# Kernel optimization log

Measured on AMD Instinct MI355X. Metric: run time of the kernel, lower is better.

The kernel has to match this reference:

```python
import jax, jax.numpy as jnp
import numpy as np

IN_DIM = 1024
OUT_DIM = 1024
NHEAD = 16
K = 9  # template(1032) - dim(1024) + 1


def _slinear(vec, template, conv_w, conv_b, lin_b):
    # Conv2d over template produces the [out_dim, in_dim] weight matrix.
    w = jax.lax.conv_general_dilated(
        template, conv_w, window_strides=(1, 1), padding='VALID',
        dimension_numbers=('NCHW', 'OIHW', 'NCHW'))  # [1,1,out_dim,in_dim]
    w = w[0, 0] + conv_b  # broadcast conv bias (scalar per out-channel)
    return vec @ w.T + lin_b  # F.linear(vec, w) + bias


def setup_inputs() -> dict:
    key = jax.random.key(0)
    ks = jax.random.split(key, 13)
    S, B = 2048, 2
    d = {
        'query': jax.random.normal(ks[0], (S, B, IN_DIM), jnp.float32),
        'key': jax.random.normal(ks[1], (S, B, IN_DIM), jnp.float32),
        'value': jax.random.normal(ks[2], (S, B, IN_DIM), jnp.float32),
        'template': jax.random.normal(ks[3], (1, 1, 1032, 1032), jnp.float32),
    }
    for i, name in enumerate(['wq', 'wk', 'wv']):
        d[name + '_cw'] = jax.random.normal(ks[4 + 3 * i], (1, 1, K, K), jnp.float32) * 0.05
        d[name + '_cb'] = jax.random.normal(ks[5 + 3 * i], (1,), jnp.float32) * 0.05
        d[name + '_b'] = jax.random.normal(ks[6 + 3 * i], (OUT_DIM,), jnp.float32) * 0.05
    return d


def reference(query, key, value, template,
              wq_cw, wq_cb, wq_b, wk_cw, wk_cb, wk_b, wv_cw, wv_cb, wv_b):
    q = _slinear(query, template, wq_cw, wq_cb, wq_b)
    k = _slinear(key, template, wk_cw, wk_cb, wk_b)
    v = _slinear(value, template, wv_cw, wv_cb, wv_b)
    S, B = q.shape[0], q.shape[1]
    h_dim = OUT_DIM // NHEAD
    scale = h_dim ** 0.5
    qh = q.reshape(S, B, NHEAD, h_dim)
    kh = k.reshape(S, B, NHEAD, h_dim)
    vh = v.reshape(S, B, NHEAD, h_dim)
    # batch_first=False path: scores then softmax over last dim
    scores = jnp.einsum('ibhd,jbhd->bhij', qh, kh) / scale  # [B,H,S,S]
    attn = jax.nn.softmax(scores, axis=-1)
    out = jnp.einsum('bhij,jbhd->ibhd', attn, vh).reshape(S, B, OUT_DIM)
    return out
```

## Files before the change

### kernel.cpp

```cpp
#include <hip/hip_runtime.h>
#include <math.h>

#define TDIM   1032
#define DIM    1024
#define SLEN   2048
#define BATCH  2
#define NROWS  (SLEN*BATCH)
#define NHEAD  16
#define HD     64

typedef unsigned short u16;
typedef short short8 __attribute__((ext_vector_type(8)));
typedef short bf16x4 __attribute__((ext_vector_type(4)));
typedef float f32x4  __attribute__((ext_vector_type(4)));

#define CSCALE 0.18033688011112042f

__device__ inline unsigned fbits(float x) {
    union { float f; unsigned u; } v; v.f = x; return v.u;
}
__device__ inline float asfloat(unsigned u) {
    union { unsigned u; float f; } v; v.u = u; return v.f;
}
__device__ inline u16 f2bf_rne(float x) {
    unsigned u = fbits(x);
    unsigned r = u + 0x7fffu + ((u >> 16) & 1u);
    return (u16)(r >> 16);
}
__device__ inline float bf2f(u16 b) { return asfloat(((unsigned)b) << 16); }
__device__ inline void dma16(const u16* g, u16* l) {
    __builtin_amdgcn_global_load_lds(
        (const __attribute__((address_space(1))) void*)g,
        (__attribute__((address_space(3))) void*)l, 16, 0, 0);
}

__global__ __launch_bounds__(256) void conv_weight_kernel(
    const float* __restrict__ tmpl,
    const float* __restrict__ cw0, const float* __restrict__ cb0,
    const float* __restrict__ cw1, const float* __restrict__ cb1,
    const float* __restrict__ cw2, const float* __restrict__ cb2,
    u16* __restrict__ Wh, u16* __restrict__ Wl)
{
    int t = blockIdx.z;
    const float* cw = (t == 0) ? cw0 : ((t == 1) ? cw1 : cw2);
    const float* cb = (t == 0) ? cb0 : ((t == 1) ? cb1 : cb2);
    __shared__ float scw[81];
    if (threadIdx.x < 81) scw[threadIdx.x] = cw[threadIdx.x];
    __syncthreads();
    int i = blockIdx.x * 256 + threadIdx.x;
    int o4 = blockIdx.y * 4;
    float cbv = cb[0];
    float acc[4] = {cbv, cbv, cbv, cbv};
    #pragma unroll
    for (int ry = 0; ry < 12; ++ry) {
        const float* trow = tmpl + (size_t)(o4 + ry) * TDIM + i;
        float tv[9];
        #pragma unroll
        for (int dx = 0; dx < 9; ++dx) tv[dx] = trow[dx];
        #pragma unroll
        for (int oo = 0; oo < 4; ++oo) {
            int dy = ry - oo;
            if (dy >= 0 && dy <= 8) {
                #pragma unroll
                for (int dx = 0; dx < 9; ++dx)
                    acc[oo] = fmaf(scw[dy * 9 + dx], tv[dx], acc[oo]);
            }
        }
    }
    #pragma unroll
    for (int oo = 0; oo < 4; ++oo) {
        size_t idx = (size_t)t * DIM * DIM + (size_t)(o4 + oo) * DIM + i;
        u16 h = f2bf_rne(acc[oo]);
        Wh[idx] = h;
        Wl[idx] = f2bf_rne(acc[oo] - bf2f(h));
    }
}

__global__ __launch_bounds__(256) void xsplit_kernel(
    const float* __restrict__ x0, const float* __restrict__ x1,
    const float* __restrict__ x2,
    u16* __restrict__ Xh, u16* __restrict__ Xl)
{
    int t = blockIdx.y;
    const float* X = (t == 0) ? x0 : ((t == 1) ? x1 : x2);
    u16* oh = Xh + (size_t)t * NROWS * DIM;
    u16* ol = Xl + (size_t)t * NROWS * DIM;
    size_t base = ((size_t)blockIdx.x * 256 + threadIdx.x) * 8;
    float4 a = *(const float4*)(X + base);
    float4 b = *(const float4*)(X + base + 4);
    float v[8] = {a.x, a.y, a.z, a.w, b.x, b.y, b.z, b.w};
    short8 hv, lv;
    #pragma unroll
    for (int e = 0; e < 8; ++e) {
        unsigned u = fbits(v[e]);
        hv[e] = (short)(u >> 16);
        float l = v[e] - asfloat(u & 0xffff0000u);
        lv[e] = (short)(fbits(l) >> 16);
    }
    *(short8*)(oh + base) = hv;
    *(short8*)(ol + base) = lv;
}

__global__ __launch_bounds__(256, 3) void qkv_mfma_gemm_ps(
    const u16* __restrict__ Xhg, const u16* __restrict__ Xlg,
    const u16* __restrict__ Whg, const u16* __restrict__ Wlg,
    const float* __restrict__ b0, const float* __restrict__ b1,
    const float* __restrict__ b2,
    u16* __restrict__ Qh, u16* __restrict__ Ql,
    u16* __restrict__ Kh, u16* __restrict__ Kl,
    u16* __restrict__ Vb)
{
    unsigned flat = blockIdx.x + 8u * blockIdx.y + 256u * blockIdx.z;
    unsigned swz = (flat & 7u) * 96u + (flat >> 3);
    int t = swz >> 8;
    int n0 = (swz & 7u) * 128;
    int m0 = ((swz >> 3) & 31u) * 128;

    const u16* Ah_g = Xhg + (size_t)t * NROWS * DIM;
    const u16* Al_g = Xlg + (size_t)t * NROWS * DIM;
    const u16* Bh_g = Whg + (size_t)t * DIM * DIM;
    const u16* Bl_g = Wlg + (size_t)t * DIM * DIM;
    const float* bias = (t == 0) ? b0 : ((t == 1) ? b1 : b2);

    __shared__ __align__(16) u16 lds[16384];
    u16* sAh = lds;
    u16* sAl = lds + 4096;
    u16* sBh = lds + 8192;
    u16* sBl = lds + 12288;

    int tid = threadIdx.x;
    int w = tid >> 6, lane = tid & 63;
    int c = lane & 15, quad = lane >> 4;
    int mh = (w >> 1) * 64, nh = (w & 1) * 64;

    int srow = lane >> 2, sgr = lane & 3;
    int ssw = sgr ^ ((srow >> 1) & 3);

    f32x4 acc[4][4];
    #pragma unroll
    for (int i = 0; i < 4; ++i)
        #pragma unroll
        for (int j = 0; j < 4; ++j)
            #pragma unroll
            for (int r = 0; r < 4; ++r) acc[i][j][r] = 0.0f;

    float bias_v[4];
    #pragma unroll
    for (int tn = 0; tn < 4; ++tn) bias_v[tn] = bias[n0 + nh + tn * 16 + c];

    #define STAGE(kg) do {                                                     \
        _Pragma("unroll")                                                      \
        for (int i_ = 0; i_ < 2; ++i_) {                                       \
            int rb = w * 32 + i_ * 16;                                         \
            size_t ro = (size_t)(n0 + rb + srow) * DIM + ((kg) + ssw) * 8;     \
            dma16(Bh_g + ro, sBh + rb * 32);                                   \
            dma16(Bl_g + ro, sBl + rb * 32);                                   \
            size_t ao = (size_t)(m0 + rb + srow) * DIM + ((kg) + ssw) * 8;     \
            dma16(Ah_g + ao, sAh + rb * 32);                                   \
            dma16(Al_g + ao, sAl + rb * 32);                                   \
        }                                                                      \
    } while (0)

    STAGE(0);

    for (int it = 0; it < 32; ++it) {
        __syncthreads();

        short8 ah[4], al[4], bh[4], bl[4];
        int rsw = (quad ^ ((c >> 1) & 3)) * 8;
        #pragma unroll
        for (int tt = 0; tt < 4; ++tt) {
            int mi = (mh + tt * 16 + c) * 32 + rsw;
            ah[tt] = *(short8*)(sAh + mi);
            al[tt] = *(short8*)(sAl + mi);
            int ni = (nh + tt * 16 + c) * 32 + rsw;
            bh[tt] = *(short8*)(sBh + ni);
            bl[tt] = *(short8*)(sBl + ni);
        }
        __syncthreads();

        if (it < 31) STAGE((it + 1) * 4);

        #pragma unroll
        for (int tm = 0; tm < 4; ++tm)
            #pragma unroll
            for (int tn = 0; tn < 4; ++tn) {
                acc[tm][tn] = __builtin_amdgcn_mfma_f32_16x16x32_bf16(
                    ah[tm], bh[tn], acc[tm][tn], 0, 0, 0);
                acc[tm][tn] = __builtin_amdgcn_mfma_f32_16x16x32_bf16(
                    ah[tm], bl[tn], acc[tm][tn], 0, 0, 0);
                acc[tm][tn] = __builtin_amdgcn_mfma_f32_16x16x32_bf16(
                    al[tm], bh[tn], acc[tm][tn], 0, 0, 0);
            }
    }
    #undef STAGE

    if (t < 2) {
        u16* Yh = (t == 0) ? Qh : Kh;
        u16* Yl = (t == 0) ? Ql : Kl;
        float qs = (t == 0) ? CSCALE : 1.0f;
        #pragma unroll
        for (int tm = 0; tm < 4; ++tm)
            #pragma unroll
            for (int r = 0; r < 4; ++r) {
                int m = m0 + mh + tm * 16 + quad * 4 + r;
                #pragma unroll
                for (int tn = 0; tn < 4; ++tn) {
                    int n = n0 + nh + tn * 16 + c;
                    float o = (acc[tm][tn][r] + bias_v[tn]) * qs;
                    unsigned bo = fbits(o);
                    Yh[(size_t)m * DIM + n] = (u16)(bo >> 16);
                    float l = o - asfloat(bo & 0xffff0000u);
                    Yl[(size_t)m * DIM + n] = (u16)(fbits(l) >> 16);
                }
            }
    } else {
        #pragma unroll
        for (int tm = 0; tm < 4; ++tm)
            #pragma unroll
            for (int r = 0; r < 4; ++r) {
                int m = m0 + mh + tm * 16 + quad * 4 + r;
                #pragma unroll
                for (int tn = 0; tn < 4; ++tn) {
                    int n = n0 + nh + tn * 16 + c;
                    Vb[(size_t)m * DIM + n] =
                        (u16)(fbits(acc[tm][tn][r] + bias_v[tn]) >> 16);
                }
            }
    }
}

__global__ __launch_bounds__(256, 3) void qkv_mfma_gemm_fb(
    const float* __restrict__ x0, const float* __restrict__ x1,
    const float* __restrict__ x2,
    const u16* __restrict__ Whg, const u16* __restrict__ Wlg,
    const float* __restrict__ b0, const float* __restrict__ b1,
    const float* __restrict__ b2,
    u16* __restrict__ Qh, u16* __restrict__ Ql,
    u16* __restrict__ Kh, u16* __restrict__ Kl,
    u16* __restrict__ Vb)
{
    unsigned flat = blockIdx.x + 8u * blockIdx.y + 256u * blockIdx.z;
    unsigned swz = (flat & 7u) * 96u + (flat >> 3);
    int t = swz >> 8;
    int n0 = (swz & 7u) * 128;
    int m0 = ((swz >> 3) & 31u) * 128;

    const float* X    = (t == 0) ? x0 : ((t == 1) ? x1 : x2);
    const u16* Bh_g   = Whg + (size_t)t * DIM * DIM;
    const u16* Bl_g   = Wlg + (size_t)t * DIM * DIM;
    const float* bias = (t == 0) ? b0 : ((t == 1) ? b1 : b2);

    __shared__ __align__(16) u16 lds[16384];
    u16* sAh = lds;
    u16* sAl = lds + 4096;
    u16* sBh = lds + 8192;
    u16* sBl = lds + 12288;

    int tid = threadIdx.x;
    int w = tid >> 6, lane = tid & 63;
    int c = lane & 15, quad = lane >> 4;
    int mh = (w >> 1) * 64, nh = (w & 1) * 64;

    int arow = w * 32 + (lane & 31);
    int acol = (lane >> 5) * 16;
    const float* aptr = X + (size_t)(m0 + arow) * DIM + acol;
    int awz = (arow >> 1) & 3;

    int srow = lane >> 2, sgr = lane & 3;
    int bsw = sgr ^ ((srow >> 1) & 3);

    f32x4 acc[4][4];
    #pragma unroll
    for (int i = 0; i < 4; ++i)
        #pragma unroll
        for (int j = 0; j < 4; ++j)
            #pragma unroll
            for (int r = 0; r < 4; ++r) acc[i][j][r] = 0.0f;

    float bias_v[4];
    #pragma unroll
    for (int tn = 0; tn < 4; ++tn) bias_v[tn] = bias[n0 + nh + tn * 16 + c];

    float4 xa[4];
    #pragma unroll
    for (int i = 0; i < 2; ++i) {
        int rb = w * 32 + i * 16;
        const u16* gh = Bh_g + (size_t)(n0 + rb + srow) * DIM + bsw * 8;
        const u16* gl = Bl_g + (size_t)(n0 + rb + srow) * DIM + bsw * 8;
        dma16(gh, sBh + rb * 32);
        dma16(gl, sBl + rb * 32);
    }
    #pragma unroll
    for (int j = 0; j < 4; ++j) xa[j] = *(const float4*)(aptr + j * 4);

    for (int it = 0; it < 32; ++it) {
        #pragma unroll
        for (int g = 0; g < 2; ++g) {
            float v[8] = { xa[2*g].x, xa[2*g].y, xa[2*g].z, xa[2*g].w,
                           xa[2*g+1].x, xa[2*g+1].y, xa[2*g+1].z, xa[2*g+1].w };
            short8 hv, lv;
            #pragma unroll
            for (int e = 0; e < 8; ++e) {
                unsigned u = fbits(v[e]);
                hv[e] = (short)(u >> 16);
                float l = v[e] - asfloat(u & 0xffff0000u);
                lv[e] = (short)(fbits(l) >> 16);
            }
            int chunk = (((lane >> 5) * 2 + g) ^ awz) * 8;
            *(short8*)(sAh + arow * 32 + chunk) = hv;
            *(short8*)(sAl + arow * 32 + chunk) = lv;
        }
        __syncthreads();

        short8 ah[4], al[4], bh[4], bl[4];
        int rsw = (quad ^ ((c >> 1) & 3)) * 8;
        #pragma unroll
        for (int tt = 0; tt < 4; ++tt) {
            int mi = (mh + tt * 16 + c) * 32 + rsw;
            ah[tt] = *(short8*)(sAh + mi);
            al[tt] = *(short8*)(sAl + mi);
            int ni = (nh + tt * 16 + c) * 32 + rsw;
            bh[tt] = *(short8*)(sBh + ni);
            bl[tt] = *(short8*)(sBl + ni);
        }
        __syncthreads();

        if (it < 31) {
            int kg = (it + 1) * 4;
            #pragma unroll
            for (int i = 0; i < 2; ++i) {
                int rb = w * 32 + i * 16;
                const u16* gh = Bh_g + (size_t)(n0 + rb + srow) * DIM + (kg + bsw) * 8;
                const u16* gl = Bl_g + (size_t)(n0 + rb + srow) * DIM + (kg + bsw) * 8;
                dma16(gh, sBh + rb * 32);
                dma16(gl, sBl + rb * 32);
            }
            #pragma unroll
            for (int j = 0; j < 4; ++j)
                xa[j] = *(const float4*)(aptr + (it + 1) * 32 + j * 4);
        }

        #pragma unroll
        for (int tm = 0; tm < 4; ++tm)
            #pragma unroll
            for (int tn = 0; tn < 4; ++tn) {
                acc[tm][tn] = __builtin_amdgcn_mfma_f32_16x16x32_bf16(
                    ah[tm], bh[tn], acc[tm][tn], 0, 0, 0);
                acc[tm][tn] = __builtin_amdgcn_mfma_f32_16x16x32_bf16(
                    ah[tm], bl[tn], acc[tm][tn], 0, 0, 0);
                acc[tm][tn] = __builtin_amdgcn_mfma_f32_16x16x32_bf16(
                    al[tm], bh[tn], acc[tm][tn], 0, 0, 0);
            }
    }

    if (t < 2) {
        u16* Yh = (t == 0) ? Qh : Kh;
        u16* Yl = (t == 0) ? Ql : Kl;
        float qs = (t == 0) ? CSCALE : 1.0f;
        #pragma unroll
        for (int tm = 0; tm < 4; ++tm)
            #pragma unroll
            for (int r = 0; r < 4; ++r) {
                int m = m0 + mh + tm * 16 + quad * 4 + r;
                #pragma unroll
                for (int tn = 0; tn < 4; ++tn) {
                    int n = n0 + nh + tn * 16 + c;
                    float o = (acc[tm][tn][r] + bias_v[tn]) * qs;
                    unsigned bo = fbits(o);
                    Yh[(size_t)m * DIM + n] = (u16)(bo >> 16);
                    float l = o - asfloat(bo & 0xffff0000u);
                    Yl[(size_t)m * DIM + n] = (u16)(fbits(l) >> 16);
                }
            }
    } else {
        #pragma unroll
        for (int tm = 0; tm < 4; ++tm)
            #pragma unroll
            for (int r = 0; r < 4; ++r) {
                int m = m0 + mh + tm * 16 + quad * 4 + r;
                #pragma unroll
                for (int tn = 0; tn < 4; ++tn) {
                    int n = n0 + nh + tn * 16 + c;
                    Vb[(size_t)m * DIM + n] =
                        (u16)(fbits(acc[tm][tn][r] + bias_v[tn]) >> 16);
                }
            }
    }
}

__global__ __launch_bounds__(256) void vt_kernel(
    const u16* __restrict__ Vb, u16* __restrict__ Vt)
{
    int b = blockIdx.z, h = blockIdx.y, s0 = blockIdx.x * 64;
    __shared__ __align__(16) u16 tile[64][80];
    int tid = threadIdx.x;
    int sl = tid >> 2, d0 = (tid & 3) * 16;
    const u16* src = Vb + (size_t)((s0 + sl) * BATCH + b) * DIM + h * HD + d0;
    short8 v0 = *(const short8*)src;
    short8 v1 = *(const short8*)(src + 8);
    #pragma unroll
    for (int j = 0; j < 8; ++j) {
        tile[d0 + j][sl] = (u16)v0[j];
        tile[d0 + 8 + j][sl] = (u16)v1[j];
    }
    __syncthreads();
    int d = tid >> 2, sc0 = (tid & 3) * 16;
    u16* dst = Vt + (size_t)((b * NHEAD + h) * HD + d) * SLEN + s0 + sc0;
    *(short8*)dst = *(const short8*)&tile[d][sc0];
    *(short8*)(dst + 8) = *(const short8*)&tile[d][sc0 + 8];
}

__global__ __launch_bounds__(512, 4) void attn_mfma_kernel(
    const u16* __restrict__ Qh, const u16* __restrict__ Ql,
    const u16* __restrict__ Kh, const u16* __restrict__ Kl,
    const u16* __restrict__ Vt, float* __restrict__ out)
{
    unsigned flat = blockIdx.x + 16u * blockIdx.y + 256u * blockIdx.z;
    unsigned swz = (flat & 7u) * 64u + (flat >> 3);
    int q0 = (swz & 15u) * 128;
    int h = (swz >> 4) & 15u;
    int b = swz >> 8;

    int tid = threadIdx.x;
    int w = tid >> 6, lane = tid & 63;
    int c = lane & 15, quad = lane >> 4;

    __shared__ __align__(16) u16 sbuf[2][3][4096];
    __shared__ __align__(16) u16 sP[8][1024];

    short8 qhf[2], qlf[2];
    {
        int s = q0 + w * 16 + c;
        size_t base = (size_t)(s * BATCH + b) * DIM + h * HD + quad * 8;
        qhf[0] = *(const short8*)(Qh + base);
        qhf[1] = *(const short8*)(Qh + base + 32);
        qlf[0] = *(const short8*)(Ql + base);
        qlf[1] = *(const short8*)(Ql + base + 32);
    }

    f32x4 acc[4];
    #pragma unroll
    for (int i = 0; i < 4; ++i)
        #pragma unroll
        for (int r = 0; r < 4; ++r) acc[i][r] = 0.0f;
    float m_run = -1e38f, l_run = 0.0f;

    int r3 = lane >> 3, c3 = lane & 7;
    int sw = c3 ^ r3;
    const size_t bhofs = (size_t)(b * NHEAD + h) * HD;

    #define ISSUE_DMA(n0v, bufv) do {                                          \
        int row_ = w * 8 + r3;                                                 \
        size_t gk = (size_t)(((n0v) + row_) * BATCH + b) * DIM + h * HD + sw * 8; \
        dma16(Kh + gk, &sbuf[bufv][0][w * 512]);                               \
        dma16(Kl + gk, &sbuf[bufv][1][w * 512]);                               \
        size_t gv = (bhofs + row_) * SLEN + (n0v) + sw * 8;                    \
        dma16(Vt + gv, &sbuf[bufv][2][w * 512]);                               \
    } while (0)

    ISSUE_DMA(0, 0);

    for (int it = 0; it < 32; ++it) {
        int cur = it & 1;
        __syncthreads();
        if (it < 31) ISSUE_DMA((it + 1) * 64, cur ^ 1);

        const u16* bKh = sbuf[cur][0];
        const u16* bKl = sbuf[cur][1];
        const u16* bVt = sbuf[cur][2];

        f32x4 sc[4];
        #pragma unroll
        for (int ct = 0; ct < 4; ++ct) {
            int row = ct * 16 + c, rw = row & 7;
            int kb = row * 64;
            short8 kh0 = *(const short8*)(bKh + kb + ((quad ^ rw) * 8));
            short8 kh1 = *(const short8*)(bKh + kb + (((4 + quad) ^ rw) * 8));
            short8 kl0 = *(const short8*)(bKl + kb + ((quad ^ rw) * 8));
            short8 kl1 = *(const short8*)(bKl + kb + (((4 + quad) ^ rw) * 8));
            __builtin_amdgcn_s_setprio(1);
            f32x4 s = {0.0f, 0.0f, 0.0f, 0.0f};
            s = __builtin_amdgcn_mfma_f32_16x16x32_bf16(kh0, qhf[0], s, 0, 0, 0);
            s = __builtin_amdgcn_mfma_f32_16x16x32_bf16(kh1, qhf[1], s, 0, 0, 0);
            s = __builtin_amdgcn_mfma_f32_16x16x32_bf16(kh0, qlf[0], s, 0, 0, 0);
            s = __builtin_amdgcn_mfma_f32_16x16x32_bf16(kh1, qlf[1], s, 0, 0, 0);
            s = __builtin_amdgcn_mfma_f32_16x16x32_bf16(kl0, qhf[0], s, 0, 0, 0);
            s = __builtin_amdgcn_mfma_f32_16x16x32_bf16(kl1, qhf[1], s, 0, 0, 0);
            __builtin_amdgcn_s_setprio(0);
            sc[ct] = s;
        }

        short8 vv[4][2];
        #pragma unroll
        for (int ctd = 0; ctd < 4; ++ctd) {
            int vrow = ctd * 16 + c, vrw = vrow & 7;
            int vb = vrow * 64;
            vv[ctd][0] = *(const short8*)(bVt + vb + ((quad ^ vrw) * 8));
            vv[ctd][1] = *(const short8*)(bVt + vb + (((4 + quad) ^ vrw) * 8));
        }

        u16* wp = sP[w];
        short8 pf0, pf1;
        {
            float m00 = fmaxf(fmaxf(sc[0][0], sc[0][1]), fmaxf(sc[0][2], sc[0][3]));
            float m01 = fmaxf(fmaxf(sc[1][0], sc[1][1]), fmaxf(sc[1][2], sc[1][3]));
            float m10 = fmaxf(fmaxf(sc[2][0], sc[2][1]), fmaxf(sc[2][2], sc[2][3]));
            float m11 = fmaxf(fmaxf(sc[3][0], sc[3][1]), fmaxf(sc[3][2], sc[3][3]));
            float pm = fmaxf(fmaxf(m00, m01), fmaxf(m10, m11));
            pm = fmaxf(pm, __shfl_xor(pm, 16));
            pm = fmaxf(pm, __shfl_xor(pm, 32));
            float mnew = fmaxf(m_run, pm);
            bool noresc = __all(pm <= m_run);
            if (!noresc) {
                float al = exp2f(m_run - mnew);
                float alr[4];
                #pragma unroll
                for (int r = 0; r < 4; ++r)
                    alr[r] = __shfl(al, (lane & 48) | (quad * 4 + r));
                #pragma unroll
                for (int ctd = 0; ctd < 4; ++ctd)
                    #pragma unroll
                    for (int r = 0; r < 4; ++r) acc[ctd][r] *= alr[r];
                l_run *= al;
            }
            m_run = mnew;

            float psp[4];
            int prow = c * 64;
            #pragma unroll
            for (int ct = 0; ct < 4; ++ct) {
                float p0 = exp2f(sc[ct][0] - mnew);
                float p1 = exp2f(sc[ct][1] - mnew);
                float p2 = exp2f(sc[ct][2] - mnew);
                float p3 = exp2f(sc[ct][3] - mnew);
                psp[ct] = (p0 + p1) + (p2 + p3);
                bf16x4 pk;
                pk[0] = (short)(fbits(p0) >> 16);
                pk[1] = (short)(fbits(p1) >> 16);
                pk[2] = (short)(fbits(p2) >> 16);
                pk[3] = (short)(fbits(p3) >> 16);
                int phys = (ct * 2 + (quad >> 1)) ^ (c & 7);
                *(bf16x4*)(wp + prow + phys * 8 + (quad & 1) * 4) = pk;
            }
            float ps = (psp[0] + psp[1]) + (psp[2] + psp[3]);
            ps += __shfl_xor(ps, 16);
            ps += __shfl_xor(ps, 32);
            l_run += ps;

            int rw = c & 7;
            pf0 = *(const short8*)(wp + prow + ((quad ^ rw) * 8));
            pf1 = *(const short8*)(wp + prow + (((4 + quad) ^ rw) * 8));
        }

        __builtin_amdgcn_s_setprio(1);
        #pragma unroll
        for (int ctd = 0; ctd < 4; ++ctd) {
            acc[ctd] = __builtin_amdgcn_mfma_f32_16x16x32_bf16(
                pf0, vv[ctd][0], acc[ctd], 0, 0, 0);
            acc[ctd] = __builtin_amdgcn_mfma_f32_16x16x32_bf16(
                pf1, vv[ctd][1], acc[ctd], 0, 0, 0);
        }
        __builtin_amdgcn_s_setprio(0);
    }
    #undef ISSUE_DMA

    {
        float rl[4];
        #pragma unroll
        for (int r = 0; r < 4; ++r)
            rl[r] = 1.0f / __shfl(l_run, (lane & 48) | (quad * 4 + r));
        #pragma unroll
        for (int ctd = 0; ctd < 4; ++ctd)
            #pragma unroll
            for (int r = 0; r < 4; ++r) {
                int s = q0 + w * 16 + quad * 4 + r;
                out[(size_t)(s * BATCH + b) * DIM + h * HD + ctd * 16 + c] =
                    acc[ctd][r] * rl[r];
            }
    }
}

extern "C" void kernel_launch(void* const* d_in, const int* in_sizes, int n_in,
                              void* d_out, int out_size, void* d_ws, size_t ws_size,
                              hipStream_t stream)
{
    const float* query = (const float*)d_in[0];
    const float* key_  = (const float*)d_in[1];
    const float* value = (const float*)d_in[2];
    const float* tmpl  = (const float*)d_in[3];
    const float* wq_cw = (const float*)d_in[4];
    const float* wq_cb = (const float*)d_in[5];
    const float* wq_b  = (const float*)d_in[6];
    const float* wk_cw = (const float*)d_in[7];
    const float* wk_cb = (const float*)d_in[8];
    const float* wk_b  = (const float*)d_in[9];
    const float* wv_cw = (const float*)d_in[10];
    const float* wv_cb = (const float*)d_in[11];
    const float* wv_b  = (const float*)d_in[12];

    char* ws = (char*)d_ws;
    u16* Wh = (u16*)(ws);
    u16* Wl = (u16*)(ws + 6291456);
    u16* Qh = (u16*)(ws + 12582912);
    u16* Ql = (u16*)(ws + 20971520);
    u16* Kh = (u16*)(ws + 29360128);
    u16* Kl = (u16*)(ws + 37748736);
    u16* Vb = (u16*)(ws + 46137344);
    u16* Vt = (u16*)(ws + 54525952);
    u16* Xh = (u16*)(ws + 62914560);
    u16* Xl = (u16*)(ws + 88080384);
    float* out = (float*)d_out;

    bool presplit = ws_size >= 113246208ull;

    conv_weight_kernel<<<dim3(DIM / 256, DIM / 4, 3), 256, 0, stream>>>(
        tmpl, wq_cw, wq_cb, wk_cw, wk_cb, wv_cw, wv_cb, Wh, Wl);

    if (presplit) {
        xsplit_kernel<<<dim3(NROWS * DIM / (256 * 8), 3), 256, 0, stream>>>(
            query, key_, value, Xh, Xl);
        qkv_mfma_gemm_ps<<<dim3(DIM / 128, NROWS / 128, 3), 256, 0, stream>>>(
            Xh, Xl, Wh, Wl, wq_b, wk_b, wv_b, Qh, Ql, Kh, Kl, Vb);
    } else {
        qkv_mfma_gemm_fb<<<dim3(DIM / 128, NROWS / 128, 3), 256, 0, stream>>>(
            query, key_, value, Wh, Wl, wq_b, wk_b, wv_b, Qh, Ql, Kh, Kl, Vb);
    }

    vt_kernel<<<dim3(SLEN / 64, NHEAD, BATCH), 256, 0, stream>>>(Vb, Vt);

    attn_mfma_kernel<<<dim3(SLEN / 128, NHEAD, BATCH), 512, 0, stream>>>(
        Qh, Ql, Kh, Kl, Vt, out);
}
```

Baseline: 300.3 us.

## Process two query sub-tiles per warp in attention to reuse K/V fragments

Each warp now handles 32 query rows (two 16-row sub-tiles) instead of 16, so the attention block covers 256 queries and the grid halves. Every K and V fragment loaded from shared memory, and every K/V DMA tile, now feeds twice as many MFMAs. This cuts K/V traffic per query and doubles per-warp instruction-level parallelism. In exchange, register use roughly doubles for accumulators, scores and Q fragments, launch bounds drop to 2 blocks per CU, and there are only 256 blocks for the GPU's CUs.

Result: slower. 314.9 us (+4.9%).

```diff
diff --git a/kernel.cpp b/kernel.cpp
--- a/kernel.cpp
+++ b/kernel.cpp
@@ -411,40 +411,43 @@
     *(short8*)(dst + 8) = *(const short8*)&tile[d][sc0 + 8];
 }
 
-__global__ __launch_bounds__(512, 4) void attn_mfma_kernel(
+__global__ __launch_bounds__(512, 2) void attn_mfma_kernel(
     const u16* __restrict__ Qh, const u16* __restrict__ Ql,
     const u16* __restrict__ Kh, const u16* __restrict__ Kl,
     const u16* __restrict__ Vt, float* __restrict__ out)
 {
-    unsigned flat = blockIdx.x + 16u * blockIdx.y + 256u * blockIdx.z;
-    unsigned swz = (flat & 7u) * 64u + (flat >> 3);
-    int q0 = (swz & 15u) * 128;
-    int h = (swz >> 4) & 15u;
-    int b = swz >> 8;
+    unsigned flat = blockIdx.x + 8u * blockIdx.y + 128u * blockIdx.z;
+    unsigned swz = (flat & 7u) * 32u + (flat >> 3);
+    int q0 = (swz & 7u) * 256;
+    int h = (swz >> 3) & 15u;
+    int b = swz >> 7;
 
     int tid = threadIdx.x;
     int w = tid >> 6, lane = tid & 63;
     int c = lane & 15, quad = lane >> 4;
 
     __shared__ __align__(16) u16 sbuf[2][3][4096];
-    __shared__ __align__(16) u16 sP[8][1024];
-
-    short8 qhf[2], qlf[2];
-    {
-        int s = q0 + w * 16 + c;
+    __shared__ __align__(16) u16 sP[8][2048];
+
+    short8 qhf[2][2], qlf[2][2];
+    #pragma unroll
+    for (int u = 0; u < 2; ++u) {
+        int s = q0 + w * 32 + u * 16 + c;
         size_t base = (size_t)(s * BATCH + b) * DIM + h * HD + quad * 8;
-        qhf[0] = *(const short8*)(Qh + base);
-        qhf[1] = *(const short8*)(Qh + base + 32);
-        qlf[0] = *(const short8*)(Ql + base);
-        qlf[1] = *(const short8*)(Ql + base + 32);
-    }
-
-    f32x4 acc[4];
-    #pragma unroll
-    for (int i = 0; i < 4; ++i)
-        #pragma unroll
-        for (int r = 0; r < 4; ++r) acc[i][r] = 0.0f;
-    float m_run = -1e38f, l_run = 0.0f;
+        qhf[u][0] = *(const short8*)(Qh + base);
+        qhf[u][1] = *(const short8*)(Qh + base + 32);
+        qlf[u][0] = *(const short8*)(Ql + base);
+        qlf[u][1] = *(const short8*)(Ql + base + 32);
+    }
+
+    f32x4 acc[2][4];
+    #pragma unroll
+    for (int u = 0; u < 2; ++u)
+        #pragma unroll
+        for (int i = 0; i < 4; ++i)
+            #pragma unroll
+            for (int r = 0; r < 4; ++r) acc[u][i][r] = 0.0f;
+    float m_run[2] = {-1e38f, -1e38f}, l_run[2] = {0.0f, 0.0f};
 
     int r3 = lane >> 3, c3 = lane & 7;
     int sw = c3 ^ r3;
@@ -470,7 +473,7 @@
         const u16* bKl = sbuf[cur][1];
         const u16* bVt = sbuf[cur][2];
 
-        f32x4 sc[4];
+        f32x4 sc[2][4];
         #pragma unroll
         for (int ct = 0; ct < 4; ++ct) {
             int row = ct * 16 + c, rw = row & 7;
@@ -480,15 +483,18 @@
             short8 kl0 = *(const short8*)(bKl + kb + ((quad ^ rw) * 8));
             short8 kl1 = *(const short8*)(bKl + kb + (((4 + quad) ^ rw) * 8));
             __builtin_amdgcn_s_setprio(1);
-            f32x4 s = {0.0f, 0.0f, 0.0f, 0.0f};
-            s = __builtin_amdgcn_mfma_f32_16x16x32_bf16(kh0, qhf[0], s, 0, 0, 0);
-            s = __builtin_amdgcn_mfma_f32_16x16x32_bf16(kh1, qhf[1], s, 0, 0, 0);
-            s = __builtin_amdgcn_mfma_f32_16x16x32_bf16(kh0, qlf[0], s, 0, 0, 0);
-            s = __builtin_amdgcn_mfma_f32_16x16x32_bf16(kh1, qlf[1], s, 0, 0, 0);
-            s = __builtin_amdgcn_mfma_f32_16x16x32_bf16(kl0, qhf[0], s, 0, 0, 0);
-            s = __builtin_amdgcn_mfma_f32_16x16x32_bf16(kl1, qhf[1], s, 0, 0, 0);
+            #pragma unroll
+            for (int u = 0; u < 2; ++u) {
+                f32x4 s = {0.0f, 0.0f, 0.0f, 0.0f};
+                s = __builtin_amdgcn_mfma_f32_16x16x32_bf16(kh0, qhf[u][0], s, 0, 0, 0);
+                s = __builtin_amdgcn_mfma_f32_16x16x32_bf16(kh1, qhf[u][1], s, 0, 0, 0);
+                s = __builtin_amdgcn_mfma_f32_16x16x32_bf16(kh0, qlf[u][0], s, 0, 0, 0);
+                s = __builtin_amdgcn_mfma_f32_16x16x32_bf16(kh1, qlf[u][1], s, 0, 0, 0);
+                s = __builtin_amdgcn_mfma_f32_16x16x32_bf16(kl0, qhf[u][0], s, 0, 0, 0);
+                s = __builtin_amdgcn_mfma_f32_16x16x32_bf16(kl1, qhf[u][1], s, 0, 0, 0);
+                sc[u][ct] = s;
+            }
             __builtin_amdgcn_s_setprio(0);
-            sc[ct] = s;
         }
 
         short8 vv[4][2];
@@ -501,19 +507,20 @@
         }
 
         u16* wp = sP[w];
-        short8 pf0, pf1;
-        {
-            float m00 = fmaxf(fmaxf(sc[0][0], sc[0][1]), fmaxf(sc[0][2], sc[0][3]));
-            float m01 = fmaxf(fmaxf(sc[1][0], sc[1][1]), fmaxf(sc[1][2], sc[1][3]));
-            float m10 = fmaxf(fmaxf(sc[2][0], sc[2][1]), fmaxf(sc[2][2], sc[2][3]));
-            float m11 = fmaxf(fmaxf(sc[3][0], sc[3][1]), fmaxf(sc[3][2], sc[3][3]));
+        short8 pf[2][2];
+        #pragma unroll
+        for (int u = 0; u < 2; ++u) {
+            float m00 = fmaxf(fmaxf(sc[u][0][0], sc[u][0][1]), fmaxf(sc[u][0][2], sc[u][0][3]));
+            float m01 = fmaxf(fmaxf(sc[u][1][0], sc[u][1][1]), fmaxf(sc[u][1][2], sc[u][1][3]));
+            float m10 = fmaxf(fmaxf(sc[u][2][0], sc[u][2][1]), fmaxf(sc[u][2][2], sc[u][2][3]));
+            float m11 = fmaxf(fmaxf(sc[u][3][0], sc[u][3][1]), fmaxf(sc[u][3][2], sc[u][3][3]));
             float pm = fmaxf(fmaxf(m00, m01), fmaxf(m10, m11));
             pm = fmaxf(pm, __shfl_xor(pm, 16));
             pm = fmaxf(pm, __shfl_xor(pm, 32));
-            float mnew = fmaxf(m_run, pm);
-            bool noresc = __all(pm <= m_run);
+            float mnew = fmaxf(m_run[u], pm);
+            bool noresc = __all(pm <= m_run[u]);
             if (!noresc) {
-                float al = exp2f(m_run - mnew);
+                float al = exp2f(m_run[u] - mnew);
                 float alr[4];
                 #pragma unroll
                 for (int r = 0; r < 4; ++r)
@@ -521,19 +528,19 @@
                 #pragma unroll
                 for (int ctd = 0; ctd < 4; ++ctd)
                     #pragma unroll
-                    for (int r = 0; r < 4; ++r) acc[ctd][r] *= alr[r];
-                l_run *= al;
-            }
-            m_run = mnew;
+                    for (int r = 0; r < 4; ++r) acc[u][ctd][r] *= alr[r];
+                l_run[u] *= al;
+            }
+            m_run[u] = mnew;
 
             float psp[4];
-            int prow = c * 64;
+            int prow = (u * 16 + c) * 64;
             #pragma unroll
             for (int ct = 0; ct < 4; ++ct) {
-                float p0 = exp2f(sc[ct][0] - mnew);
-                float p1 = exp2f(sc[ct][1] - mnew);
-                float p2 = exp2f(sc[ct][2] - mnew);
-                float p3 = exp2f(sc[ct][3] - mnew);
+                float p0 = exp2f(sc[u][ct][0] - mnew);
+                float p1 = exp2f(sc[u][ct][1] - mnew);
+                float p2 = exp2f(sc[u][ct][2] - mnew);
+                float p3 = exp2f(sc[u][ct][3] - mnew);
                 psp[ct] = (p0 + p1) + (p2 + p3);
                 bf16x4 pk;
                 pk[0] = (short)(fbits(p0) >> 16);
@@ -546,37 +553,41 @@
             float ps = (psp[0] + psp[1]) + (psp[2] + psp[3]);
             ps += __shfl_xor(ps, 16);
             ps += __shfl_xor(ps, 32);
-            l_run += ps;
+            l_run[u] += ps;
 
             int rw = c & 7;
-            pf0 = *(const short8*)(wp + prow + ((quad ^ rw) * 8));
-            pf1 = *(const short8*)(wp + prow + (((4 + quad) ^ rw) * 8));
+            pf[u][0] = *(const short8*)(wp + prow + ((quad ^ rw) * 8));
+            pf[u][1] = *(const short8*)(wp + prow + (((4 + quad) ^ rw) * 8));
         }
 
         __builtin_amdgcn_s_setprio(1);
         #pragma unroll
         for (int ctd = 0; ctd < 4; ++ctd) {
-            acc[ctd] = __builtin_amdgcn_mfma_f32_16x16x32_bf16(
-                pf0, vv[ctd][0], acc[ctd], 0, 0, 0);
-            acc[ctd] = __builtin_amdgcn_mfma_f32_16x16x32_bf16(
-                pf1, vv[ctd][1], acc[ctd], 0, 0, 0);
+            #pragma unroll
+            for (int u = 0; u < 2; ++u) {
+                acc[u][ctd] = __builtin_amdgcn_mfma_f32_16x16x32_bf16(
+                    pf[u][0], vv[ctd][0], acc[u][ctd], 0, 0, 0);
+                acc[u][ctd] = __builtin_amdgcn_mfma_f32_16x16x32_bf16(
+                    pf[u][1], vv[ctd][1], acc[u][ctd], 0, 0, 0);
+            }
         }
         __builtin_amdgcn_s_setprio(0);
     }
     #undef ISSUE_DMA
 
-    {
+    #pragma unroll
+    for (int u = 0; u < 2; ++u) {
         float rl[4];
         #pragma unroll
         for (int r = 0; r < 4; ++r)
-            rl[r] = 1.0f / __shfl(l_run, (lane & 48) | (quad * 4 + r));
+            rl[r] = 1.0f / __shfl(l_run[u], (lane & 48) | (quad * 4 + r));
         #pragma unroll
         for (int ctd = 0; ctd < 4; ++ctd)
             #pragma unroll
             for (int r = 0; r < 4; ++r) {
-                int s = q0 + w * 16 + quad * 4 + r;
+                int s = q0 + w * 32 + u * 16 + quad * 4 + r;
                 out[(size_t)(s * BATCH + b) * DIM + h * HD + ctd * 16 + c] =
-                    acc[ctd][r] * rl[r];
+                    acc[u][ctd][r] * rl[r];
             }
     }
 }
@@ -629,6 +640,6 @@
 
     vt_kernel<<<dim3(SLEN / 64, NHEAD, BATCH), 256, 0, stream>>>(Vb, Vt);
 
-    attn_mfma_kernel<<<dim3(SLEN / 128, NHEAD, BATCH), 512, 0, stream>>>(
+    attn_mfma_kernel<<<dim3(SLEN / 256, NHEAD, BATCH), 512, 0, stream>>>(
         Qh, Ql, Kh, Kl, Vt, out);
 }
```
